# Performance work log

Hardware: AMD Instinct MI355X
Metric: run time of the kernel (lower is better)

## Reference

```python
import jax, jax.numpy as jnp
from jax import lax
import numpy as np

B, C, O, H, W = 4, 64, 64, 128, 128


def setup_inputs() -> dict:
    key = jax.random.key(0)
    ks = jax.random.split(key, 3)
    x = jax.random.normal(ks[0], (B, C, H, W), dtype=jnp.float32)
    # small offset-conv weights so learned offsets stay in a realistic +-few-pixel range
    offset_w = jax.random.normal(ks[1], (27, C, 3, 3), dtype=jnp.float32) * 0.01
    offset_b = jnp.zeros((27,), dtype=jnp.float32)
    dcn_w = jax.random.normal(ks[2], (O, C, 3, 3), dtype=jnp.float32) * (1.0 / np.sqrt(C * 9))
    dcn_b = jnp.zeros((O,), dtype=jnp.float32)
    gamma = jnp.ones((O,), dtype=jnp.float32)
    beta = jnp.zeros((O,), dtype=jnp.float32)
    return {"x": x, "offset_w": offset_w, "offset_b": offset_b,
            "dcn_w": dcn_w, "dcn_b": dcn_b, "gamma": gamma, "beta": beta}


def _bilinear_sample(img, y, x):
    """img: [B,C,H,W]; y,x: [B,K,H,W] fractional coords. Returns [B,C,K,H,W].
    Out-of-range corners contribute 0 (DCNv2 semantics)."""
    Bs, Cs, Hs, Ws = img.shape
    flat = img.reshape(Bs, Cs, Hs * Ws)
    y0 = jnp.floor(y)
    x0 = jnp.floor(x)
    wy = y - y0
    wx = x - x0

    def gather(yi, xi):
        valid = (yi >= 0) & (yi <= Hs - 1) & (xi >= 0) & (xi <= Ws - 1)
        yc = jnp.clip(yi, 0, Hs - 1).astype(jnp.int32)
        xc = jnp.clip(xi, 0, Ws - 1).astype(jnp.int32)
        idx = (yc * Ws + xc).reshape(Bs, -1)  # [B, K*H*W]
        v = jax.vmap(lambda f, i: jnp.take(f, i, axis=1))(flat, idx)  # [B,C,K*H*W]
        v = v.reshape(Bs, Cs, *y.shape[1:])
        return v * valid[:, None].astype(img.dtype)

    out = jnp.zeros((Bs, Cs) + y.shape[1:], dtype=img.dtype)
    for dy, dx in ((0, 0), (0, 1), (1, 0), (1, 1)):
        w = (wy if dy else 1.0 - wy) * (wx if dx else 1.0 - wx)
        out = out + gather(y0 + dy, x0 + dx) * w[:, None]
    return out


def reference(x, offset_w, offset_b, dcn_w, dcn_b, gamma, beta):
    Bs, Cs, Hs, Ws = x.shape
    Os = dcn_w.shape[0]
    # offset-predicting 3x3 conv, stride 1, pad 1
    om = lax.conv_general_dilated(
        x, offset_w, window_strides=(1, 1), padding=((1, 1), (1, 1)),
        dimension_numbers=("NCHW", "OIHW", "NCHW")) + offset_b[None, :, None, None]
    off_x, off_y, mask = jnp.split(om, 3, axis=1)  # each [B,9,H,W]
    mask = jax.nn.sigmoid(mask)

    # base sampling grid: p0 + kernel tap offset (stride 1, pad 1, dil 1)
    ky, kx = jnp.meshgrid(jnp.arange(3), jnp.arange(3), indexing="ij")
    kyf = ky.reshape(9).astype(x.dtype)
    kxf = kx.reshape(9).astype(x.dtype)
    hh = jnp.arange(Hs, dtype=x.dtype)
    ww = jnp.arange(Ws, dtype=x.dtype)
    py = hh[None, None, :, None] - 1.0 + kyf[None, :, None, None] + off_y  # [B,9,H,W]
    px = ww[None, None, None, :] - 1.0 + kxf[None, :, None, None] + off_x  # [B,9,H,W]

    sampled = _bilinear_sample(x, py, px)          # [B,C,9,H,W]
    sampled = sampled * mask[:, None]              # sigmoid modulation
    out = jnp.einsum("bckhw,ock->bohw", sampled, dcn_w.reshape(Os, Cs, 9))
    out = out + dcn_b[None, :, None, None]

    # BatchNorm (training-mode batch stats) + ReLU
    mu = out.mean(axis=(0, 2, 3), keepdims=True)
    var = out.var(axis=(0, 2, 3), keepdims=True)
    out = (out - mu) * lax.rsqrt(var + 1e-5)
    out = out * gamma[None, :, None, None] + beta[None, :, None, None]
    return jax.nn.relu(out)
```

## Files before the change

### kernel.cpp

```cpp
#include <hip/hip_runtime.h>
#include <math.h>

#define Hh 128
#define Ww 128
#define HW (Hh*Ww)
#define Bn 4
#define Cn 64
#define On 64
#define KP 200
#define OMP 66
#define NBLK 1024

typedef __attribute__((ext_vector_type(8))) short bf16x8;
typedef __attribute__((ext_vector_type(4))) float f32x4;
typedef __attribute__((ext_vector_type(4))) unsigned short u16x4;
typedef __attribute__((ext_vector_type(2))) unsigned u32x2;
typedef __attribute__((ext_vector_type(4))) unsigned u32x4;

static __device__ __forceinline__ unsigned short f2bf(float f) {
    unsigned u = __builtin_bit_cast(unsigned, f);
    u += 0x7FFFu + ((u >> 16) & 1u);
    return (unsigned short)(u >> 16);
}
static __device__ __forceinline__ short f2h(float f) {
    _Float16 h = (_Float16)f;
    return __builtin_bit_cast(short, h);
}
static __device__ __forceinline__ float h2f(short s) {
    return (float)__builtin_bit_cast(_Float16, s);
}
static __device__ __forceinline__ float bflo(unsigned d) {
    return __builtin_bit_cast(float, d << 16);
}
static __device__ __forceinline__ float bfhi(unsigned d) {
    return __builtin_bit_cast(float, d & 0xFFFF0000u);
}

#define XTB_BYTES   ((size_t)Bn*HW*64*2)
#define CONV_BYTES  ((size_t)Bn*On*HW*4)
#define PART_BYTES  ((size_t)128*NBLK*4)

__global__ __launch_bounds__(256) void prep_k(
    const float* __restrict__ x,  const float* __restrict__ ow,
    const float* __restrict__ dw, unsigned* __restrict__ xtb,
    short* __restrict__ owT,      short* __restrict__ dwT)
{
    int blk = blockIdx.x;
    int t = threadIdx.x;
    if (blk < 512) {
        int b = blk >> 7, h = blk & 127;
        __shared__ float sT[64 * 133];
        const float* xp = x + (size_t)b * Cn * HW + (size_t)h * Ww;
#pragma unroll
        for (int it = 0; it < 32; ++it) {
            int idx = t + 256 * it;
            int c = idx >> 7, w = idx & 127;
            sT[c * 133 + w] = xp[(size_t)c * HW + w];
        }
        __syncthreads();
        unsigned* op = xtb + (size_t)blk * Ww * 32;
#pragma unroll
        for (int it = 0; it < 16; ++it) {
            int idx = t + 256 * it;
            int w = idx >> 5, cp = idx & 31;
            unsigned lo = f2bf(sT[(2 * cp) * 133 + w]);
            unsigned hi = f2bf(sT[(2 * cp + 1) * 133 + w]);
            op[(size_t)w * 32 + cp] = lo | (hi << 16);
        }
    } else {
        int u = (blk - 512) * 4 + (t >> 6);
        int c = t & 63;
        if (u < 288) {
            int o = u / 9, kk = u % 9;
            float v = (o < 27) ? ow[(size_t)o * 576 + c * 9 + kk] : 0.0f;
            owT[(size_t)u * 64 + c] = (short)f2bf(v);
        } else {
            int u2 = u - 288;
            int o = u2 / 9, kk = u2 % 9;
            dwT[(size_t)u2 * 64 + c] = (short)f2bf(dw[(size_t)o * 576 + c * 9 + kk]);
        }
    }
}

__global__ __launch_bounds__(256) void dcn_fused_k(
    const unsigned* __restrict__ xtb, const short* __restrict__ owT,
    const float* __restrict__ ob,     const short* __restrict__ dwT,
    float* __restrict__ conv,         float* __restrict__ part)
{
    int raw  = blockIdx.x;
    int blk  = ((raw & 7) << 7) | (raw >> 3);
    int half = blk & 1;
    int h    = (blk >> 1) & 127;
    int b    = blk >> 8;
    int px0  = half * 64;
    int t    = threadIdx.x;
    int lane = t & 63;
    int quad = lane >> 4;
    int l15  = lane & 15;
    int qw   = lane >> 4;
    int cl2  = lane & 15;
    int og   = lane >> 3;
    int li   = lane & 7;
    int w_s  = __builtin_amdgcn_readfirstlane(t >> 6);

    __shared__ __align__(16) short sA[64 * KP];
    __shared__ __align__(16) unsigned short prepQ[576 * 4];
    __shared__ __align__(16) unsigned short prepC[576];
    short* sOMh = sA;

    const unsigned* xbd = xtb + (size_t)b * HW * 32;
    unsigned* sAd = (unsigned*)sA;

    int nt_o = w_s & 1;
    int mh   = w_s >> 1;
    int o_ow = nt_o * 16 + l15;
    f32x4 oacc[2] = {{0,0,0,0},{0,0,0,0}};

    for (int ck = 0; ck < 3; ++ck) {
        int yy = h + ck - 1;
        bool rowok = ((unsigned)yy < (unsigned)Hh);
#pragma unroll
        for (int it = 0; it < 6; ++it) {
            int unit = (it * 4 + w_s) * 8 + og;
            int kkl = unit >> 6, px = unit & 63;
            int xx = px0 + px + kkl - 1;
            bool valid = rowok && ((unsigned)xx < (unsigned)Ww);
            u32x4 v = {0u, 0u, 0u, 0u};
            if (valid)
                v = *(const u32x4*)&xbd[(((size_t)yy << 7) + xx) * 32 + li * 4];
            *(u32x4*)&sAd[px * 100 + kkl * 32 + li * 4] = v;
        }
        __syncthreads();
#pragma unroll
        for (int ks = 0; ks < 6; ++ks) {
            int kk = ck * 3 + (ks >> 1);
            bf16x8 bfr = *(const bf16x8*)&owT[((size_t)o_ow * 9 + kk) * 64
                                             + (ks & 1) * 32 + quad * 8];
#pragma unroll
            for (int m2 = 0; m2 < 2; ++m2) {
                bf16x8 a = *(const bf16x8*)&sA[(mh * 32 + m2 * 16 + l15) * KP
                                               + ks * 32 + quad * 8];
                oacc[m2] = __builtin_amdgcn_mfma_f32_16x16x32_bf16(a, bfr, oacc[m2], 0, 0, 0);
            }
        }
        __syncthreads();
    }
    if (o_ow < 27) {
        float bias = ob[o_ow];
#pragma unroll
        for (int m2 = 0; m2 < 2; ++m2) {
            int pxb = (mh * 2 + m2) * 16 + quad * 4;
#pragma unroll
            for (int r = 0; r < 4; ++r)
                sOMh[o_ow * OMP + pxb + r] = f2h(oacc[m2][r] + bias);
        }
    }
    __syncthreads();

#pragma unroll
    for (int i = 0; i < 3; ++i) {
        int u = t + 256 * i;
        if (u < 576) {
            int kk = u >> 6, px = u & 63;
            float ox = h2f((short)sOMh[kk * OMP + px]);
            float oy = h2f((short)sOMh[(9 + kk) * OMP + px]);
            float mr = h2f((short)sOMh[(18 + kk) * OMP + px]);
            float m  = 1.0f / (1.0f + __expf(-mr));
            float py  = (float)(h - 1 + (kk / 3)) + oy;
            float pxf = (float)(px0 + px - 1 + (kk % 3)) + ox;
            float y0f = floorf(py), x0f = floorf(pxf);
            int y0 = (int)y0f, x0 = (int)x0f;
            float wy = py - y0f, wx = pxf - x0f;
            int yb = min(max(y0, 0), Hh - 2);
            int xb = min(max(x0, 0), Ww - 2);
            float wr0 = (yb == y0) ? (1.0f - wy) : ((yb     == y0 + 1) ? wy : 0.0f);
            float wr1 = (yb == y0) ? wy          : ((yb + 1 == y0    ) ? (1.0f - wy) : 0.0f);
            float wc0 = (xb == x0) ? (1.0f - wx) : ((xb     == x0 + 1) ? wx : 0.0f);
            float wc1 = (xb == x0) ? wx          : ((xb + 1 == x0    ) ? (1.0f - wx) : 0.0f);
            wr0 *= m; wr1 *= m;
            prepQ[u * 4 + 0] = (unsigned short)(yb * Ww + xb);
            prepQ[u * 4 + 1] = (unsigned short)f2h(wr0 * wc0);
            prepQ[u * 4 + 2] = (unsigned short)f2h(wr0 * wc1);
            prepQ[u * 4 + 3] = (unsigned short)f2h(wr1 * wc0);
            prepC[u]         = (unsigned short)f2h(wr1 * wc1);
        }
    }
    __syncthreads();

    int o_dw = w_s * 16 + l15;
    f32x4 acc[4] = {{0,0,0,0},{0,0,0,0},{0,0,0,0},{0,0,0,0}};

    for (int ck = 0; ck < 3; ++ck) {
#pragma unroll 4
        for (int it = 0; it < 12; ++it) {
            int unit = (it * 4 + w_s) * 4 + qw;
            int kkl = unit >> 6, px = unit & 63;
            int uG = (ck * 3 + kkl) * 64 + px;
            u16x4 q = *(const u16x4*)&prepQ[uG * 4];
            float w00 = h2f((short)q[1]);
            float w01 = h2f((short)q[2]);
            float w10 = h2f((short)q[3]);
            float w11 = h2f((short)prepC[uG]);
            const unsigned* p0 = xbd + (size_t)q[0] * 32 + cl2 * 2;
            u32x2 d00 = *(const u32x2*)(p0);
            u32x2 d01 = *(const u32x2*)(p0 + 32);
            u32x2 d10 = *(const u32x2*)(p0 + 4096);
            u32x2 d11 = *(const u32x2*)(p0 + 4128);
            u32x2 pkv;
#pragma unroll
            for (int j = 0; j < 2; ++j) {
                float v0 = w00 * bflo(d00[j]) + w01 * bflo(d01[j])
                         + w10 * bflo(d10[j]) + w11 * bflo(d11[j]);
                float v1 = w00 * bfhi(d00[j]) + w01 * bfhi(d01[j])
                         + w10 * bfhi(d10[j]) + w11 * bfhi(d11[j]);
                unsigned pk;
                asm("v_cvt_pk_bf16_f32 %0, %1, %2" : "=v"(pk) : "v"(v0), "v"(v1));
                pkv[j] = pk;
            }
            *(u32x2*)&sAd[px * 100 + kkl * 32 + cl2 * 2] = pkv;
        }
        __syncthreads();
#pragma unroll
        for (int ks = 0; ks < 6; ++ks) {
            int kk = ck * 3 + (ks >> 1);
            bf16x8 bfr = *(const bf16x8*)&dwT[((size_t)o_dw * 9 + kk) * 64
                                              + (ks & 1) * 32 + quad * 8];
#pragma unroll
            for (int mt = 0; mt < 4; ++mt) {
                bf16x8 a = *(const bf16x8*)&sA[(mt * 16 + l15) * KP
                                               + ks * 32 + quad * 8];
                acc[mt] = __builtin_amdgcn_mfma_f32_16x16x32_bf16(a, bfr, acc[mt], 0, 0, 0);
            }
        }
        __syncthreads();
    }

#pragma unroll
    for (int mt = 0; mt < 4; ++mt) {
        size_t idx = ((size_t)b * On + o_dw) * HW + (size_t)h * Ww + px0 + mt * 16 + quad * 4;
        *(f32x4*)(conv + idx) = acc[mt];
    }
    float s1 = 0.0f, s2 = 0.0f;
#pragma unroll
    for (int mt = 0; mt < 4; ++mt) {
#pragma unroll
        for (int r = 0; r < 4; ++r) {
            float v = acc[mt][r];
            s1 += v;
            s2 += v * v;
        }
    }
    s1 += __shfl_down(s1, 32, 64);  s2 += __shfl_down(s2, 32, 64);
    s1 += __shfl_down(s1, 16, 64);  s2 += __shfl_down(s2, 16, 64);
    if (lane < 16) {
        part[(size_t)o_dw * NBLK + blk]        = s1;
        part[(size_t)(64 + o_dw) * NBLK + blk] = s2;
    }
}

__global__ __launch_bounds__(256) void bnstats_k(
    const float* __restrict__ part, const float* __restrict__ gamma,
    const float* __restrict__ beta, const float* __restrict__ conv,
    float* __restrict__ out)
{
    int idx = blockIdx.x;
    int o  = idx & 63;
    int bq = idx >> 6;
    int t = threadIdx.x;
    float s1 = 0.0f, s2 = 0.0f;
#pragma unroll
    for (int i = 0; i < NBLK / 256; ++i) {
        int j = t + 256 * i;
        s1 += part[(size_t)o * NBLK + j];
        s2 += part[(size_t)(64 + o) * NBLK + j];
    }
#pragma unroll
    for (int off = 32; off > 0; off >>= 1) {
        s1 += __shfl_down(s1, off, 64);
        s2 += __shfl_down(s2, off, 64);
    }
    __shared__ float r1[4], r2[4];
    __shared__ float sc_s, sh_s;
    if ((t & 63) == 0) { r1[t >> 6] = s1; r2[t >> 6] = s2; }
    __syncthreads();
    if (t == 0) {
        float S1 = r1[0] + r1[1] + r1[2] + r1[3];
        float S2 = r2[0] + r2[1] + r2[2] + r2[3];
        float n = (float)(Bn * HW);
        float mu = S1 / n;
        float var = S2 / n - mu * mu;
        float sc = gamma[o] * rsqrtf(var + 1e-5f);
        sc_s = sc;
        sh_s = beta[o] - mu * sc;
    }
    __syncthreads();
    float sc = sc_s, sh = sh_s;
    size_t base = (((size_t)(bq >> 2) * On + o) * HW + (size_t)(bq & 3) * 4096) / 4;
    const float4* cv = (const float4*)conv + base;
    float4* ov = (float4*)out + base;
#pragma unroll
    for (int i = 0; i < 4; ++i) {
        float4 v = cv[t + 256 * i];
        v.x = fmaxf(v.x * sc + sh, 0.0f);
        v.y = fmaxf(v.y * sc + sh, 0.0f);
        v.z = fmaxf(v.z * sc + sh, 0.0f);
        v.w = fmaxf(v.w * sc + sh, 0.0f);
        ov[t + 256 * i] = v;
    }
}

extern "C" void kernel_launch(void* const* d_in, const int* in_sizes, int n_in,
                              void* d_out, int out_size, void* d_ws, size_t ws_size,
                              hipStream_t stream)
{
    const float* x     = (const float*)d_in[0];
    const float* ow    = (const float*)d_in[1];
    const float* ob    = (const float*)d_in[2];
    const float* dw    = (const float*)d_in[3];
    const float* gamma = (const float*)d_in[5];
    const float* beta  = (const float*)d_in[6];

    char* wsb = (char*)d_ws;
    unsigned* xtb = (unsigned*)wsb;
    float* conv = (float*)(wsb + XTB_BYTES);
    float* part = (float*)(wsb + XTB_BYTES + CONV_BYTES);
    short* owT  = (short*)(wsb + XTB_BYTES + CONV_BYTES + PART_BYTES + 512);
    short* dwT  = owT + 288 * 64;

    prep_k     <<<dim3(728),  dim3(256), 0, stream>>>(x, ow, dw, xtb, owT, dwT);
    dcn_fused_k<<<dim3(NBLK), dim3(256), 0, stream>>>(xtb, owT, ob, dwT, conv, part);
    bnstats_k  <<<dim3(1024), dim3(256), 0, stream>>>(part, gamma, beta, conv, (float*)d_out);
}
```

Measured before the change: 131.6 us.

## Double wavefronts per block in fused DCN kernel, splitting pixel tiles across waves

Grows the fused deformable-conv block from 4 to 8 wavefronts. Each wave now computes half as many MFMA tiles in both the offset conv and the main conv, and the gather/staging loops are split across twice as many threads. The BN partial sums get a second slot per block (NPART = 2048), and the stats kernel reads twice as many partials. The aim is more latency hiding per block for the gather-heavy phase, at the cost of each bf16 weight fragment being loaded by more waves and less MFMA work per wave.

```diff
diff --git a/kernel.cpp b/kernel.cpp
--- a/kernel.cpp
+++ b/kernel.cpp
@@ -10,6 +10,7 @@
 #define KP 200
 #define OMP 66
 #define NBLK 1024
+#define NPART 2048
 
 typedef __attribute__((ext_vector_type(8))) short bf16x8;
 typedef __attribute__((ext_vector_type(4))) float f32x4;
@@ -38,7 +39,7 @@
 
 #define XTB_BYTES   ((size_t)Bn*HW*64*2)
 #define CONV_BYTES  ((size_t)Bn*On*HW*4)
-#define PART_BYTES  ((size_t)128*NBLK*4)
+#define PART_BYTES  ((size_t)128*NPART*4)
 
 __global__ __launch_bounds__(256) void prep_k(
     const float* __restrict__ x,  const float* __restrict__ ow,
@@ -82,7 +83,7 @@
     }
 }
 
-__global__ __launch_bounds__(256) void dcn_fused_k(
+__global__ __launch_bounds__(512) void dcn_fused_k(
     const unsigned* __restrict__ xtb, const short* __restrict__ owT,
     const float* __restrict__ ob,     const short* __restrict__ dwT,
     float* __restrict__ conv,         float* __restrict__ part)
@@ -112,16 +113,16 @@
     unsigned* sAd = (unsigned*)sA;
 
     int nt_o = w_s & 1;
-    int mh   = w_s >> 1;
+    int mq   = w_s >> 1;
     int o_ow = nt_o * 16 + l15;
-    f32x4 oacc[2] = {{0,0,0,0},{0,0,0,0}};
+    f32x4 oacc = {0,0,0,0};
 
     for (int ck = 0; ck < 3; ++ck) {
         int yy = h + ck - 1;
         bool rowok = ((unsigned)yy < (unsigned)Hh);
 #pragma unroll
-        for (int it = 0; it < 6; ++it) {
-            int unit = (it * 4 + w_s) * 8 + og;
+        for (int it = 0; it < 3; ++it) {
+            int unit = (it * 8 + w_s) * 8 + og;
             int kkl = unit >> 6, px = unit & 63;
             int xx = px0 + px + kkl - 1;
             bool valid = rowok && ((unsigned)xx < (unsigned)Ww);
@@ -136,30 +137,24 @@
             int kk = ck * 3 + (ks >> 1);
             bf16x8 bfr = *(const bf16x8*)&owT[((size_t)o_ow * 9 + kk) * 64
                                              + (ks & 1) * 32 + quad * 8];
-#pragma unroll
-            for (int m2 = 0; m2 < 2; ++m2) {
-                bf16x8 a = *(const bf16x8*)&sA[(mh * 32 + m2 * 16 + l15) * KP
-                                               + ks * 32 + quad * 8];
-                oacc[m2] = __builtin_amdgcn_mfma_f32_16x16x32_bf16(a, bfr, oacc[m2], 0, 0, 0);
-            }
+            bf16x8 a = *(const bf16x8*)&sA[(mq * 16 + l15) * KP
+                                           + ks * 32 + quad * 8];
+            oacc = __builtin_amdgcn_mfma_f32_16x16x32_bf16(a, bfr, oacc, 0, 0, 0);
         }
         __syncthreads();
     }
     if (o_ow < 27) {
         float bias = ob[o_ow];
-#pragma unroll
-        for (int m2 = 0; m2 < 2; ++m2) {
-            int pxb = (mh * 2 + m2) * 16 + quad * 4;
-#pragma unroll
-            for (int r = 0; r < 4; ++r)
-                sOMh[o_ow * OMP + pxb + r] = f2h(oacc[m2][r] + bias);
-        }
+        int pxb = mq * 16 + quad * 4;
+#pragma unroll
+        for (int r = 0; r < 4; ++r)
+            sOMh[o_ow * OMP + pxb + r] = f2h(oacc[r] + bias);
     }
     __syncthreads();
 
 #pragma unroll
-    for (int i = 0; i < 3; ++i) {
-        int u = t + 256 * i;
+    for (int i = 0; i < 2; ++i) {
+        int u = t + 512 * i;
         if (u < 576) {
             int kk = u >> 6, px = u & 63;
             float ox = h2f((short)sOMh[kk * OMP + px]);
@@ -187,13 +182,14 @@
     }
     __syncthreads();
 
-    int o_dw = w_s * 16 + l15;
-    f32x4 acc[4] = {{0,0,0,0},{0,0,0,0},{0,0,0,0},{0,0,0,0}};
+    int o_dw = (w_s & 3) * 16 + l15;
+    int mh3  = w_s >> 2;
+    f32x4 acc[2] = {{0,0,0,0},{0,0,0,0}};
 
     for (int ck = 0; ck < 3; ++ck) {
-#pragma unroll 4
-        for (int it = 0; it < 12; ++it) {
-            int unit = (it * 4 + w_s) * 4 + qw;
+#pragma unroll
+        for (int it = 0; it < 6; ++it) {
+            int unit = (it * 8 + w_s) * 4 + qw;
             int kkl = unit >> 6, px = unit & 63;
             int uG = (ck * 3 + kkl) * 64 + px;
             u16x4 q = *(const u16x4*)&prepQ[uG * 4];
@@ -226,8 +222,8 @@
             bf16x8 bfr = *(const bf16x8*)&dwT[((size_t)o_dw * 9 + kk) * 64
                                               + (ks & 1) * 32 + quad * 8];
 #pragma unroll
-            for (int mt = 0; mt < 4; ++mt) {
-                bf16x8 a = *(const bf16x8*)&sA[(mt * 16 + l15) * KP
+            for (int mt = 0; mt < 2; ++mt) {
+                bf16x8 a = *(const bf16x8*)&sA[(mh3 * 32 + mt * 16 + l15) * KP
                                                + ks * 32 + quad * 8];
                 acc[mt] = __builtin_amdgcn_mfma_f32_16x16x32_bf16(a, bfr, acc[mt], 0, 0, 0);
             }
@@ -236,13 +232,14 @@
     }
 
 #pragma unroll
-    for (int mt = 0; mt < 4; ++mt) {
-        size_t idx = ((size_t)b * On + o_dw) * HW + (size_t)h * Ww + px0 + mt * 16 + quad * 4;
+    for (int mt = 0; mt < 2; ++mt) {
+        size_t idx = ((size_t)b * On + o_dw) * HW + (size_t)h * Ww
+                   + px0 + mh3 * 32 + mt * 16 + quad * 4;
         *(f32x4*)(conv + idx) = acc[mt];
     }
     float s1 = 0.0f, s2 = 0.0f;
 #pragma unroll
-    for (int mt = 0; mt < 4; ++mt) {
+    for (int mt = 0; mt < 2; ++mt) {
 #pragma unroll
         for (int r = 0; r < 4; ++r) {
             float v = acc[mt][r];
@@ -253,8 +250,8 @@
     s1 += __shfl_down(s1, 32, 64);  s2 += __shfl_down(s2, 32, 64);
     s1 += __shfl_down(s1, 16, 64);  s2 += __shfl_down(s2, 16, 64);
     if (lane < 16) {
-        part[(size_t)o_dw * NBLK + blk]        = s1;
-        part[(size_t)(64 + o_dw) * NBLK + blk] = s2;
+        part[(size_t)o_dw * NPART + blk * 2 + mh3]        = s1;
+        part[(size_t)(64 + o_dw) * NPART + blk * 2 + mh3] = s2;
     }
 }
 
@@ -269,10 +266,10 @@
     int t = threadIdx.x;
     float s1 = 0.0f, s2 = 0.0f;
 #pragma unroll
-    for (int i = 0; i < NBLK / 256; ++i) {
+    for (int i = 0; i < NPART / 256; ++i) {
         int j = t + 256 * i;
-        s1 += part[(size_t)o * NBLK + j];
-        s2 += part[(size_t)(64 + o) * NBLK + j];
+        s1 += part[(size_t)o * NPART + j];
+        s2 += part[(size_t)(64 + o) * NPART + j];
     }
 #pragma unroll
     for (int off = 32; off > 0; off >>= 1) {
@@ -328,6 +325,6 @@
     short* dwT  = owT + 288 * 64;
 
     prep_k     <<<dim3(728),  dim3(256), 0, stream>>>(x, ow, dw, xtb, owT, dwT);
-    dcn_fused_k<<<dim3(NBLK), dim3(256), 0, stream>>>(xtb, owT, ob, dwT, conv, part);
+    dcn_fused_k<<<dim3(NBLK), dim3(512), 0, stream>>>(xtb, owT, ob, dwT, conv, part);
     bnstats_k  <<<dim3(1024), dim3(256), 0, stream>>>(part, gamma, beta, conv, (float*)d_out);
 }
```

New measurement: 150.9 us. 14.6% more time.

## Prefetch next chunk's bilinear gather loads into registers across MFMA phase

Applied to the files above, without the earlier changes.

The first four gather iterations of each channel chunk are software-pipelined. Their prep entries and four corner loads from global memory are issued before the barrier of the previous chunk, so the load latency overlaps the MFMA loop. Full __syncthreads are replaced by a manual lgkmcnt wait plus s_barrier, which avoids waiting on the outstanding global loads (vmcnt) at the barrier. This costs extra VGPRs for the prefetched data and weights, which may lower occupancy. It also relies on the manual barrier being correct for the LDS reuse.

```diff
diff --git a/kernel.cpp b/kernel.cpp
--- a/kernel.cpp
+++ b/kernel.cpp
@@ -190,12 +190,48 @@
     int o_dw = w_s * 16 + l15;
     f32x4 acc[4] = {{0,0,0,0},{0,0,0,0},{0,0,0,0},{0,0,0,0}};
 
+    u32x2 pd00[4], pd01[4], pd10[4], pd11[4];
+    float pw00[4], pw01[4], pw10[4], pw11[4];
+
+#pragma unroll
+    for (int it = 0; it < 4; ++it) {
+        int unit = (it * 4 + w_s) * 4 + qw;
+        int uG = unit;
+        u16x4 q = *(const u16x4*)&prepQ[uG * 4];
+        pw00[it] = h2f((short)q[1]);
+        pw01[it] = h2f((short)q[2]);
+        pw10[it] = h2f((short)q[3]);
+        pw11[it] = h2f((short)prepC[uG]);
+        const unsigned* p0 = xbd + (size_t)q[0] * 32 + cl2 * 2;
+        pd00[it] = *(const u32x2*)(p0);
+        pd01[it] = *(const u32x2*)(p0 + 32);
+        pd10[it] = *(const u32x2*)(p0 + 4096);
+        pd11[it] = *(const u32x2*)(p0 + 4128);
+    }
+
     for (int ck = 0; ck < 3; ++ck) {
+#pragma unroll
+        for (int it = 0; it < 4; ++it) {
+            int unit = (it * 4 + w_s) * 4 + qw;
+            int px = unit & 63;
+            u32x2 pkv;
+#pragma unroll
+            for (int j = 0; j < 2; ++j) {
+                float v0 = pw00[it] * bflo(pd00[it][j]) + pw01[it] * bflo(pd01[it][j])
+                         + pw10[it] * bflo(pd10[it][j]) + pw11[it] * bflo(pd11[it][j]);
+                float v1 = pw00[it] * bfhi(pd00[it][j]) + pw01[it] * bfhi(pd01[it][j])
+                         + pw10[it] * bfhi(pd10[it][j]) + pw11[it] * bfhi(pd11[it][j]);
+                unsigned pk;
+                asm("v_cvt_pk_bf16_f32 %0, %1, %2" : "=v"(pk) : "v"(v0), "v"(v1));
+                pkv[j] = pk;
+            }
+            *(u32x2*)&sAd[px * 100 + cl2 * 2] = pkv;
+        }
 #pragma unroll 4
-        for (int it = 0; it < 12; ++it) {
+        for (int it = 4; it < 12; ++it) {
             int unit = (it * 4 + w_s) * 4 + qw;
             int kkl = unit >> 6, px = unit & 63;
-            int uG = (ck * 3 + kkl) * 64 + px;
+            int uG = ck * 192 + unit;
             u16x4 q = *(const u16x4*)&prepQ[uG * 4];
             float w00 = h2f((short)q[1]);
             float w01 = h2f((short)q[2]);
@@ -219,7 +255,25 @@
             }
             *(u32x2*)&sAd[px * 100 + kkl * 32 + cl2 * 2] = pkv;
         }
-        __syncthreads();
+        if (ck < 2) {
+#pragma unroll
+            for (int it = 0; it < 4; ++it) {
+                int unit = (it * 4 + w_s) * 4 + qw;
+                int uG = (ck + 1) * 192 + unit;
+                u16x4 q = *(const u16x4*)&prepQ[uG * 4];
+                pw00[it] = h2f((short)q[1]);
+                pw01[it] = h2f((short)q[2]);
+                pw10[it] = h2f((short)q[3]);
+                pw11[it] = h2f((short)prepC[uG]);
+                const unsigned* p0 = xbd + (size_t)q[0] * 32 + cl2 * 2;
+                pd00[it] = *(const u32x2*)(p0);
+                pd01[it] = *(const u32x2*)(p0 + 32);
+                pd10[it] = *(const u32x2*)(p0 + 4096);
+                pd11[it] = *(const u32x2*)(p0 + 4128);
+            }
+        }
+        asm volatile("s_waitcnt lgkmcnt(0)" ::: "memory");
+        __builtin_amdgcn_s_barrier();
 #pragma unroll
         for (int ks = 0; ks < 6; ++ks) {
             int kk = ck * 3 + (ks >> 1);
@@ -232,7 +286,7 @@
                 acc[mt] = __builtin_amdgcn_mfma_f32_16x16x32_bf16(a, bfr, acc[mt], 0, 0, 0);
             }
         }
-        __syncthreads();
+        __builtin_amdgcn_s_barrier();
     }
 
 #pragma unroll
```

New measurement: 132.6 us. About the same (+0.7%).
